# Kernel optimization log

Hardware: AMD Instinct MI355X
Metric: run time of the kernel (lower is better)

The kernel has to match this reference:

```python
import jax, jax.numpy as jnp
import numpy as np

D_INP=36; D_MODEL=144; NHEAD=4; NHID=128; NLAYERS=2
MAX_LEN=215; D_STATIC=9; D_PE=16; N_CLASSES=2; B=128
D_OB=D_MODEL//D_INP; GCH=MAX_LEN*D_OB; D_TR=D_MODEL+D_PE; D_FINAL=D_TR+D_INP
_EI=np.stack(np.nonzero(np.ones((D_INP,D_INP),dtype=np.int64)))  # torch.nonzero(ones).T -> all pairs
SRC_N=jnp.asarray(_EI[0]); TGT_N=jnp.asarray(_EI[1]); N_EDGE=_EI.shape[1]


def setup_inputs():
    ks=jax.random.split(jax.random.key(0),40)
    def w(i,shape,s=0.05): return jax.random.normal(ks[i],shape,jnp.float32)*s
    return {
      'src': jax.random.normal(ks[0],(MAX_LEN,B,2*D_INP),jnp.float32),
      'static': jax.random.normal(ks[1],(B,D_STATIC),jnp.float32),
      'times': jax.random.uniform(ks[2],(MAX_LEN,B),jnp.float32)*MAX_LEN,
      'lengths': jax.random.randint(ks[3],(B,),32,MAX_LEN+1),
      'R_u': w(4,(1,D_INP*D_OB)),
      'emb_w': w(5,(D_INP,D_STATIC)), 'emb_b': jnp.zeros(D_INP,jnp.float32),
      'Wv1': w(6,(GCH,GCH),1.0/np.sqrt(GCH)), 'bv1': jnp.zeros(GCH,jnp.float32),
      'Wv2': w(7,(GCH,GCH),1.0/np.sqrt(GCH)), 'bv2': jnp.zeros(GCH,jnp.float32),
      'in_proj_w': w(8,(NLAYERS,3*D_TR,D_TR)), 'in_proj_b': jnp.zeros((NLAYERS,3*D_TR),jnp.float32),
      'out_w': w(9,(NLAYERS,D_TR,D_TR)), 'out_b': jnp.zeros((NLAYERS,D_TR),jnp.float32),
      'lin1_w': w(10,(NLAYERS,NHID,D_TR)), 'lin1_b': jnp.zeros((NLAYERS,NHID),jnp.float32),
      'lin2_w': w(11,(NLAYERS,D_TR,NHID)), 'lin2_b': jnp.zeros((NLAYERS,D_TR),jnp.float32),
      'ln1_s': jnp.ones((NLAYERS,D_TR),jnp.float32), 'ln1_b': jnp.zeros((NLAYERS,D_TR),jnp.float32),
      'ln2_s': jnp.ones((NLAYERS,D_TR),jnp.float32), 'ln2_b': jnp.zeros((NLAYERS,D_TR),jnp.float32),
      'mlp1_w': w(12,(D_FINAL,D_FINAL)), 'mlp1_b': jnp.zeros(D_FINAL,jnp.float32),
      'mlp2_w': w(13,(N_CLASSES,D_FINAL)), 'mlp2_b': jnp.zeros(N_CLASSES,jnp.float32),
    }


def _seg_softmax(wgt, seg, n):
    m=jnp.full((n,),-jnp.inf,wgt.dtype).at[seg].max(wgt)
    e=jnp.exp(wgt-m[seg])
    s=jnp.zeros((n,),wgt.dtype).at[seg].add(e)
    return e/s[seg]


def _ln(x,s,b):
    mu=jnp.mean(x,-1,keepdims=True); v=jnp.var(x,-1,keepdims=True)
    return (x-mu)/jnp.sqrt(v+1e-5)*s+b


def _forward(src, static, times, R_u, emb_w, emb_b, Wv1, bv1, Wv2, bv2, in_proj_w, in_proj_b, out_w, out_b, lin1_w, lin1_b, lin2_w, lin2_b, ln1_s, ln1_b, ln2_s, ln2_b, mlp1_w, mlp1_b, mlp2_w, mlp2_b, lengths):
    T,Bb=src.shape[0],src.shape[1]
    obs=src[:,:,:D_INP]                                  # drop mask half
    h=jax.nn.relu(jnp.repeat(obs,D_OB,axis=-1)*R_u)      # h_u = relu(x_u*R_u), [T,B,144]
    ts=jnp.asarray(MAX_LEN**np.linspace(0,1,D_PE//2),jnp.float32)
    scaled=times[:,:,None]/ts
    pe=jnp.concatenate([jnp.sin(scaled),jnp.cos(scaled)],-1)  # [T,B,16]
    emb=static@emb_w.T+emb_b                             # [B,36]
    # --- Observation_progation x2 (use_beta=False): gather-softmax-scatter per sensor graph ---
    xb=h.transpose(1,0,2).reshape(Bb,T,D_INP,D_OB).transpose(0,2,1,3).reshape(Bb,D_INP,GCH)
    ew=jnp.ones((N_EDGE,),jnp.float32)                   # adj=ones -> edge_weights=1
    gamma=_seg_softmax(ew,TGT_N,D_INP)                   # softmax over edges per target node
    def prop(x_,Wv,bv):
        V=jax.nn.relu(x_@Wv.T+bv)                        # relu(lin_value(x_j))
        msgs=V[:,SRC_N,:]*gamma[None,:,None]             # gather source features per edge
        return jnp.zeros_like(x_).at[:,TGT_N,:].add(msgs)  # scatter-add to targets
    x1=prop(xb,Wv1,bv1)
    x2=prop(x1,Wv2,bv2)                                  # layer2 uses alpha1 = raw edge_weights
    alpha=jnp.broadcast_to(ew[None,:],(Bb,N_EDGE))       # alpha_all.T
    sq=jnp.sum(alpha*alpha,1)
    d2=jnp.maximum(sq[:,None]+sq[None,:]-2.0*(alpha@alpha.T),0.0)
    distance=jnp.mean(jnp.sqrt(d2))
    out=x2.reshape(Bb,D_INP,T,D_OB).transpose(2,0,1,3).reshape(T,Bb,D_INP*D_OB)
    x=jnp.concatenate([out,pe],-1)                       # [T,B,160]
    mask=jnp.arange(T)[None,:]>=lengths[:,None]          # [B,T] True = padded
    hd=D_TR//NHEAD
    for l in range(NLAYERS):                             # torch post-norm TransformerEncoderLayer
        qkv=x@in_proj_w[l].T+in_proj_b[l]
        q,k,v=jnp.split(qkv,3,-1)
        def heads(t): return t.reshape(T,Bb,NHEAD,hd).transpose(1,2,0,3)  # [B,H,T,hd]
        sc=jnp.einsum('bhqd,bhkd->bhqk',heads(q),heads(k))/np.sqrt(hd)
        sc=jnp.where(mask[:,None,None,:],jnp.float32(-1e30),sc)
        o=jnp.einsum('bhqk,bhkd->bhqd',jax.nn.softmax(sc,-1),heads(v))
        o=o.transpose(2,0,1,3).reshape(T,Bb,D_TR)@out_w[l].T+out_b[l]
        x=_ln(x+o,ln1_s[l],ln1_b[l])
        ff=jax.nn.relu(x@lin1_w[l].T+lin1_b[l])@lin2_w[l].T+lin2_b[l]
        x=_ln(x+ff,ln2_s[l],ln2_b[l])
    valid=1.0-mask.T[:,:,None].astype(x.dtype)           # [T,B,1]
    agg=jnp.sum(x*valid,0)/(lengths[:,None].astype(x.dtype)+1.0)
    feat=jnp.concatenate([agg,emb],1)                    # [B,196]
    logits=jax.nn.relu(feat@mlp1_w.T+mlp1_b)@mlp2_w.T+mlp2_b
    return logits,distance


def reference(src, static, times, lengths, R_u, emb_w, emb_b, Wv1, bv1, Wv2, bv2, in_proj_w, in_proj_b, out_w, out_b, lin1_w, lin1_b, lin2_w, lin2_b, ln1_s, ln1_b, ln2_s, ln2_b, mlp1_w, mlp1_b, mlp2_w, mlp2_b):
    return _forward(src, static, times, R_u, emb_w, emb_b, Wv1, bv1, Wv2, bv2, in_proj_w, in_proj_b, out_w, out_b, lin1_w, lin1_b, lin2_w, lin2_b, ln1_s, ln1_b, ln2_s, ln2_b, mlp1_w, mlp1_b, mlp2_w, mlp2_b, lengths)
```

## Files before the change

### kernel.cpp

```cpp
#include <hip/hip_runtime.h>
#include <math.h>

#define T_LEN 215
#define TP    224
#define B_N   128
#define DINP  36
#define D_TR  160
#define HD    40
#define D_FIN 196
#define KPG   864
#define MROW  28672

typedef __attribute__((ext_vector_type(8))) short short8v;
typedef __attribute__((ext_vector_type(4))) float f32x4;

__device__ __forceinline__ ushort f2bf(float x) {
  union { float f; unsigned u; } c; c.f = x;
  unsigned r = c.u + 0x7fffu + ((c.u >> 16) & 1u);
  return (ushort)(r >> 16);
}
__device__ __forceinline__ float bf2f(ushort h) {
  union { unsigned u; float f; } c; c.u = ((unsigned)h) << 16;
  return c.f;
}

__global__ __launch_bounds__(256) void k_prep(const float* __restrict__ Wv1,
    const float* __restrict__ Wv2, const float* __restrict__ ipw, const float* __restrict__ ow,
    const float* __restrict__ l1w, const float* __restrict__ l2w,
    ushort* __restrict__ wv1b, ushort* __restrict__ wv2b, ushort* __restrict__ ipwb,
    ushort* __restrict__ owb, ushort* __restrict__ l1wb, ushort* __restrict__ l2wb,
    float* __restrict__ v2acc, float* __restrict__ featacc, ushort* __restrict__ obuf16) {
  int i = blockIdx.x * 256 + threadIdx.x;
  if (i < 746496) { int n = i / KPG, k = i % KPG;
    wv1b[i] = (n < 860 && k < 860) ? f2bf(Wv1[n * 860 + k]) : (ushort)0; return; }
  i -= 746496;
  if (i < 746496) { int n = i / KPG, k = i % KPG;
    wv2b[i] = (n < 860 && k < 860) ? f2bf(Wv2[n * 860 + k]) : (ushort)0; return; }
  i -= 746496;
  if (i < 153600) { ipwb[i] = f2bf(ipw[i]); return; }
  i -= 153600;
  if (i < 51200)  { owb[i] = f2bf(ow[i]); return; }
  i -= 51200;
  if (i < 40960)  { l1wb[i] = f2bf(l1w[i]); return; }
  i -= 40960;
  if (i < 40960)  { l2wb[i] = f2bf(l2w[i]); return; }
  i -= 40960;
  if (i < 110592) { v2acc[i] = 0.f; return; }
  i -= 110592;
  if (i < 25088)  { featacc[i] = 0.f; return; }
  i -= 25088;
  if (i < 184320) {
    int b = i / 1440, rem = i % 1440;
    int t = 215 + rem / 160, cc = rem % 160;
    obuf16[((size_t)b * TP + t) * D_TR + cc] = 0; return;
  }
}

__global__ __launch_bounds__(256) void k_xb16(const float* __restrict__ src,
    const float* __restrict__ R_u, ushort* __restrict__ xb16) {
  __shared__ float Ss[T_LEN * DINP];
  const int b = blockIdx.x, tid = threadIdx.x;
  for (int i = tid; i < T_LEN * DINP; i += 256) {
    int t = i / DINP, j = i - t * DINP;
    Ss[i] = src[((size_t)t * B_N + b) * 72 + j];
  }
  __syncthreads();
  for (int i = tid; i < DINP * T_LEN; i += 256) {
    int ii = i / T_LEN, t = i - ii * T_LEN;
    float v = Ss[t * DINP + ii];
    float4 r = ((const float4*)R_u)[ii];
    ushort4 o;
    o.x = f2bf(fmaxf(v * r.x, 0.f)); o.y = f2bf(fmaxf(v * r.y, 0.f));
    o.z = f2bf(fmaxf(v * r.z, 0.f)); o.w = f2bf(fmaxf(v * r.w, 0.f));
    ushort* row = xb16 + (size_t)(b * DINP + ii) * KPG;
    *(ushort4*)(row + 4 * t) = o;
    if (t == 0) { ushort4 z = {0, 0, 0, 0}; *(ushort4*)(row + 860) = z; }
  }
}

__global__ __launch_bounds__(256) void k_red_s1(const ushort* __restrict__ V1b, ushort* __restrict__ s1) {
  int idx = blockIdx.x * 256 + threadIdx.x;
  if (idx >= B_N * KPG) return;
  int b = idx / KPG, n = idx % KPG;
  float s = 0.f;
  if (n < 860) {
    #pragma unroll 4
    for (int i = 0; i < DINP; i++) s += bf2f(V1b[((size_t)b * DINP + i) * 860 + n]);
    s *= (1.0f / 36.0f);
  }
  s1[idx] = (n < 860) ? f2bf(s) : (ushort)0;
}

__global__ __launch_bounds__(256) void k_buildx(const float* __restrict__ v2acc,
    const float* __restrict__ bv2, const float* __restrict__ times,
    float* __restrict__ x, ushort* __restrict__ x16) {
  int idx = blockIdx.x * 256 + threadIdx.x;
  if (idx >= B_N * TP * 40) return;
  int c = idx % 40;
  int r = idx / 40;
  int t = r % TP, b = r / TP;
  float4 f = {0.f, 0.f, 0.f, 0.f};
  if (t < T_LEN) {
    if (c < 36) {
      float4 a = *(const float4*)&v2acc[(size_t)b * KPG + 4 * t];
      float4 bb = *(const float4*)&bv2[4 * t];
      f.x = fmaxf(a.x + bb.x, 0.f); f.y = fmaxf(a.y + bb.y, 0.f);
      f.z = fmaxf(a.z + bb.z, 0.f); f.w = fmaxf(a.w + bb.w, 0.f);
    } else {
      float tm = times[t * B_N + b];
      int j0 = (c - 36) * 4;
      bool is_sin = j0 < 8;
      int kb = j0 & 7;
      float o[4];
      #pragma unroll
      for (int qq = 0; qq < 4; qq++) {
        float ts = expf((float)(kb + qq) * 0.76723400f);
        float sc = tm / ts;
        o[qq] = is_sin ? sinf(sc) : cosf(sc);
      }
      f.x = o[0]; f.y = o[1]; f.z = o[2]; f.w = o[3];
    }
  }
  ((float4*)(x + (size_t)r * D_TR))[c] = f;
  ushort4 h = {f2bf(f.x), f2bf(f.y), f2bf(f.z), f2bf(f.w)};
  *(ushort4*)(x16 + (size_t)r * D_TR + 4 * c) = h;
}

template <int RELU, int SPLIT, int WMODE, int BNT>
__global__ __launch_bounds__(256) void gemm_bf16(const ushort* __restrict__ A,
    const ushort* __restrict__ W, const float* __restrict__ bias, void* __restrict__ Cv,
    int KP, int ldc, int ncols, int kts) {
  __shared__ ushort As[128 * 32];
  __shared__ ushort Ws[BNT * 32];
  constexpr int NJ = BNT / 16;
  const int tid = threadIdx.x;
  const int wave = tid >> 6, lane = tid & 63;
  const int lr = lane & 15, hi = lane >> 4;
  const int m0 = blockIdx.y * 128, n0 = blockIdx.x * BNT;
  const int kt0 = blockIdx.z * kts;

  f32x4 acc[2][NJ];
  #pragma unroll
  for (int i = 0; i < 2; i++)
    #pragma unroll
    for (int j = 0; j < NJ; j++) acc[i][j] = (f32x4){0.f, 0.f, 0.f, 0.f};

  const int ar = tid >> 2, g = tid & 3;
  const size_t abase0 = (size_t)(m0 + ar) * KP;
  const size_t abase1 = (size_t)(m0 + ar + 64) * KP;
  const size_t bbase0 = (size_t)(n0 + ar) * KP;
  const size_t bbase1 = (size_t)(n0 + ar + 64) * KP;
  const int awb0 = ar * 64 + ((g * 16) ^ ((ar & 3) << 4));
  const int awb1 = awb0 + 64 * 64;

  const int arow0 = wave * 32 + lr;
  const int arb0 = arow0 * 64 + ((hi * 16) ^ ((arow0 & 3) << 4));
  const int arb1 = (arow0 + 16) * 64 + ((hi * 16) ^ (((arow0 + 16) & 3) << 4));
  int brb[NJ];
  #pragma unroll
  for (int j = 0; j < NJ; j++)
    brb[j] = (j * 16 + lr) * 64 + ((hi * 16) ^ ((lr & 3) << 4));

  for (int kt = 0; kt < kts; ++kt) {
    const int k0 = (kt0 + kt) * 32;
    uint4 va0 = *(const uint4*)(A + abase0 + k0 + g * 8);
    uint4 va1 = *(const uint4*)(A + abase1 + k0 + g * 8);
    uint4 vb0 = *(const uint4*)(W + bbase0 + k0 + g * 8);
    uint4 vb1;
    if constexpr (BNT == 128) vb1 = *(const uint4*)(W + bbase1 + k0 + g * 8);
    if (kt) __syncthreads();
    *(uint4*)((char*)As + awb0) = va0;
    *(uint4*)((char*)As + awb1) = va1;
    *(uint4*)((char*)Ws + awb0) = vb0;
    if constexpr (BNT == 128) *(uint4*)((char*)Ws + awb1) = vb1;
    __syncthreads();
    short8v a0 = *(const short8v*)((const char*)As + arb0);
    short8v a1 = *(const short8v*)((const char*)As + arb1);
    #pragma unroll
    for (int j = 0; j < NJ; j++) {
      short8v bf = *(const short8v*)((const char*)Ws + brb[j]);
      acc[0][j] = __builtin_amdgcn_mfma_f32_16x16x32_bf16(a0, bf, acc[0][j], 0, 0, 0);
      acc[1][j] = __builtin_amdgcn_mfma_f32_16x16x32_bf16(a1, bf, acc[1][j], 0, 0, 0);
    }
  }

  #pragma unroll
  for (int i = 0; i < 2; i++) {
    #pragma unroll
    for (int j = 0; j < NJ; j++) {
      int col = n0 + j * 16 + lr;
      int row = m0 + wave * 32 + i * 16 + hi * 4;
      if (col < ncols) {
        if (SPLIT) {
          #pragma unroll
          for (int r = 0; r < 4; r++)
            atomicAdd((float*)Cv + (size_t)(row + r) * ldc + col, acc[i][j][r]);
        } else {
          float bb = bias ? bias[col] : 0.f;
          #pragma unroll
          for (int r = 0; r < 4; r++) {
            float xv = acc[i][j][r] + bb;
            if (RELU) xv = fmaxf(xv, 0.f);
            if (WMODE == 0) ((float*)Cv)[(size_t)(row + r) * ldc + col] = xv;
            else            ((ushort*)Cv)[(size_t)(row + r) * ldc + col] = f2bf(xv);
          }
        }
      }
    }
  }
}

__global__ __launch_bounds__(256) void gemm_qkv(const ushort* __restrict__ A,
    const ushort* __restrict__ W, const float* __restrict__ bias,
    ushort* __restrict__ qkvB, ushort* __restrict__ Vt, int kts) {
  __shared__ ushort As[128 * 32];
  __shared__ ushort Ws[128 * 32];
  const int KP = 160;
  const int tid = threadIdx.x;
  const int wave = tid >> 6, lane = tid & 63;
  const int lr = lane & 15, hi = lane >> 4;
  const int m0 = blockIdx.y * 128, n0 = blockIdx.x * 128;

  f32x4 acc[2][8];
  #pragma unroll
  for (int i = 0; i < 2; i++)
    #pragma unroll
    for (int j = 0; j < 8; j++) acc[i][j] = (f32x4){0.f, 0.f, 0.f, 0.f};

  const int ar = tid >> 2, g = tid & 3;
  const size_t abase0 = (size_t)(m0 + ar) * KP;
  const size_t abase1 = (size_t)(m0 + ar + 64) * KP;
  const size_t bbase0 = (size_t)(n0 + ar) * KP;
  const size_t bbase1 = (size_t)(n0 + ar + 64) * KP;
  const int awb0 = ar * 64 + ((g * 16) ^ ((ar & 3) << 4));
  const int awb1 = awb0 + 64 * 64;

  const int arow0 = wave * 32 + lr;
  const int arb0 = arow0 * 64 + ((hi * 16) ^ ((arow0 & 3) << 4));
  const int arb1 = (arow0 + 16) * 64 + ((hi * 16) ^ (((arow0 + 16) & 3) << 4));
  int brb[8];
  #pragma unroll
  for (int j = 0; j < 8; j++)
    brb[j] = (j * 16 + lr) * 64 + ((hi * 16) ^ ((lr & 3) << 4));

  for (int kt = 0; kt < kts; ++kt) {
    const int k0 = kt * 32;
    uint4 va0 = *(const uint4*)(A + abase0 + k0 + g * 8);
    uint4 va1 = *(const uint4*)(A + abase1 + k0 + g * 8);
    uint4 vb0 = *(const uint4*)(W + bbase0 + k0 + g * 8);
    uint4 vb1 = *(const uint4*)(W + bbase1 + k0 + g * 8);
    if (kt) __syncthreads();
    *(uint4*)((char*)As + awb0) = va0;
    *(uint4*)((char*)As + awb1) = va1;
    *(uint4*)((char*)Ws + awb0) = vb0;
    *(uint4*)((char*)Ws + awb1) = vb1;
    __syncthreads();
    short8v a0 = *(const short8v*)((const char*)As + arb0);
    short8v a1 = *(const short8v*)((const char*)As + arb1);
    #pragma unroll
    for (int j = 0; j < 8; j++) {
      short8v bf = *(const short8v*)((const char*)Ws + brb[j]);
      acc[0][j] = __builtin_amdgcn_mfma_f32_16x16x32_bf16(a0, bf, acc[0][j], 0, 0, 0);
      acc[1][j] = __builtin_amdgcn_mfma_f32_16x16x32_bf16(a1, bf, acc[1][j], 0, 0, 0);
    }
  }

  #pragma unroll
  for (int i = 0; i < 2; i++) {
    const int row = m0 + wave * 32 + i * 16 + hi * 4;
    const int b = row / TP, t0 = row - b * TP;
    #pragma unroll
    for (int j = 0; j < 8; j++) {
      int col = n0 + j * 16 + lr;
      if (col < 320) {
        float bb = bias[col];
        #pragma unroll
        for (int r = 0; r < 4; r++)
          qkvB[(size_t)(row + r) * 480 + col] = f2bf(acc[i][j][r] + bb);
      } else if (col < 480) {
        float bb = bias[col];
        int dg = col - 320;
        int hh = dg / 40, dd = dg - hh * 40;
        ushort4 pv;
        pv.x = f2bf(acc[i][j][0] + bb); pv.y = f2bf(acc[i][j][1] + bb);
        pv.z = f2bf(acc[i][j][2] + bb); pv.w = f2bf(acc[i][j][3] + bb);
        *(ushort4*)(Vt + (((size_t)(b * 4 + hh) * 48 + dd) * TP + t0)) = pv;
      }
    }
  }
}

__global__ __launch_bounds__(256) void gemm_ln(const ushort* __restrict__ A,
    const ushort* __restrict__ W, const float* __restrict__ bias,
    const float* __restrict__ gam, const float* __restrict__ bet,
    float* __restrict__ x, ushort* __restrict__ x16, int KP, int kts) {
  __shared__ ushort As[64 * 32];
  __shared__ ushort Ws[160 * 32];
  const int tid = threadIdx.x;
  const int wave = tid >> 6, lane = tid & 63;
  const int lr = lane & 15, hi = lane >> 4;
  const int m0 = blockIdx.x * 64;

  f32x4 acc[10];
  #pragma unroll
  for (int j = 0; j < 10; j++) acc[j] = (f32x4){0.f, 0.f, 0.f, 0.f};

  const int ar = tid >> 2, g = tid & 3;
  const size_t abase = (size_t)(m0 + ar) * KP;
  const int awb = ar * 64 + ((g * 16) ^ ((ar & 3) << 4));
  const int wr0 = tid >> 2,         ws0 = tid & 3;
  const int wr1 = (tid + 256) >> 2, ws1 = (tid + 256) & 3;
  const int wr2 = (tid + 512) >> 2, ws2 = (tid + 512) & 3;
  const int wwb0 = wr0 * 64 + ((ws0 * 16) ^ ((wr0 & 3) << 4));
  const int wwb1 = wr1 * 64 + ((ws1 * 16) ^ ((wr1 & 3) << 4));
  const int wwb2 = wr2 * 64 + ((ws2 * 16) ^ ((wr2 & 3) << 4));

  const int arow = wave * 16 + lr;
  const int arb = arow * 64 + ((hi * 16) ^ ((arow & 3) << 4));
  int brb[10];
  #pragma unroll
  for (int j = 0; j < 10; j++)
    brb[j] = (j * 16 + lr) * 64 + ((hi * 16) ^ ((lr & 3) << 4));

  for (int kt = 0; kt < kts; ++kt) {
    const int k0 = kt * 32;
    uint4 va = *(const uint4*)(A + abase + k0 + g * 8);
    uint4 w0 = *(const uint4*)(W + (size_t)wr0 * KP + k0 + ws0 * 8);
    uint4 w1 = *(const uint4*)(W + (size_t)wr1 * KP + k0 + ws1 * 8);
    uint4 w2;
    if (tid < 128) w2 = *(const uint4*)(W + (size_t)wr2 * KP + k0 + ws2 * 8);
    if (kt) __syncthreads();
    *(uint4*)((char*)As + awb) = va;
    *(uint4*)((char*)Ws + wwb0) = w0;
    *(uint4*)((char*)Ws + wwb1) = w1;
    if (tid < 128) *(uint4*)((char*)Ws + wwb2) = w2;
    __syncthreads();
    short8v a0 = *(const short8v*)((const char*)As + arb);
    #pragma unroll
    for (int j = 0; j < 10; j++) {
      short8v bf = *(const short8v*)((const char*)Ws + brb[j]);
      acc[j] = __builtin_amdgcn_mfma_f32_16x16x32_bf16(a0, bf, acc[j], 0, 0, 0);
    }
  }

  const int rb = m0 + wave * 16 + hi * 4;
  float s[4] = {0.f, 0.f, 0.f, 0.f};
  #pragma unroll
  for (int j = 0; j < 10; j++) {
    const int col = j * 16 + lr;
    const float bb = bias[col];
    #pragma unroll
    for (int r = 0; r < 4; r++) {
      float v = acc[j][r] + bb + x[(size_t)(rb + r) * D_TR + col];
      acc[j][r] = v;
      s[r] += v;
    }
  }
  #pragma unroll
  for (int r = 0; r < 4; r++) {
    s[r] += __shfl_xor(s[r], 1, 64);
    s[r] += __shfl_xor(s[r], 2, 64);
    s[r] += __shfl_xor(s[r], 4, 64);
    s[r] += __shfl_xor(s[r], 8, 64);
  }
  float mu[4], q2[4] = {0.f, 0.f, 0.f, 0.f};
  #pragma unroll
  for (int r = 0; r < 4; r++) mu[r] = s[r] * (1.0f / 160.0f);
  #pragma unroll
  for (int j = 0; j < 10; j++)
    #pragma unroll
    for (int r = 0; r < 4; r++) {
      float d = acc[j][r] - mu[r];
      q2[r] += d * d;
    }
  #pragma unroll
  for (int r = 0; r < 4; r++) {
    q2[r] += __shfl_xor(q2[r], 1, 64);
    q2[r] += __shfl_xor(q2[r], 2, 64);
    q2[r] += __shfl_xor(q2[r], 4, 64);
    q2[r] += __shfl_xor(q2[r], 8, 64);
  }
  float rstd[4];
  #pragma unroll
  for (int r = 0; r < 4; r++) rstd[r] = rsqrtf(q2[r] * (1.0f / 160.0f) + 1e-5f);
  #pragma unroll
  for (int j = 0; j < 10; j++) {
    const int col = j * 16 + lr;
    const float gc = gam[col], bc = bet[col];
    #pragma unroll
    for (int r = 0; r < 4; r++) {
      float o = (acc[j][r] - mu[r]) * rstd[r] * gc + bc;
      x[(size_t)(rb + r) * D_TR + col] = o;
      x16[(size_t)(rb + r) * D_TR + col] = f2bf(o);
    }
  }
}

__global__ __launch_bounds__(64) void k_attn4(const ushort* __restrict__ qkvB,
    const ushort* __restrict__ Vt, const int* __restrict__ lengths,
    ushort* __restrict__ o16) {
  __shared__ ushort SP[16 * 232];
  const int bh = blockIdx.x;
  const int b = bh >> 2, h = bh & 3;
  int L = lengths[b]; if (L > T_LEN) L = T_LEN;
  const int q0 = blockIdx.y << 4;
  if (q0 >= L) return;
  const int lane = threadIdx.x;
  const int lr = lane & 15, hi = lane >> 4;
  const int nk16 = (L + 15) >> 4;
  const int nkt  = (L + 31) >> 5;
  const float SC = 0.15811388300841898f;

  const ushort* qrow = qkvB + ((size_t)b * TP + q0) * 480 + h * 40;
  uint4 qa0u = *(const uint4*)(qrow + lr * 480 + hi * 8);
  uint4 qa1u = {0, 0, 0, 0};
  if (hi == 0) qa1u = *(const uint4*)(qrow + lr * 480 + 32);
  short8v qa0 = *(short8v*)&qa0u;
  short8v qa1 = *(short8v*)&qa1u;

  f32x4 c[14];
  #pragma unroll
  for (int kt = 0; kt < 14; ++kt) {
    c[kt] = (f32x4){0.f, 0.f, 0.f, 0.f};
    if (kt < nk16) {
      const ushort* krow = qkvB + ((size_t)b * TP + kt * 16) * 480 + 160 + h * 40;
      uint4 kb0u = *(const uint4*)(krow + lr * 480 + hi * 8);
      uint4 kb1u = {0, 0, 0, 0};
      if (hi == 0) kb1u = *(const uint4*)(krow + lr * 480 + 32);
      c[kt] = __builtin_amdgcn_mfma_f32_16x16x32_bf16(qa0, *(short8v*)&kb0u, c[kt], 0, 0, 0);
      c[kt] = __builtin_amdgcn_mfma_f32_16x16x32_bf16(qa1, *(short8v*)&kb1u, c[kt], 0, 0, 0);
    }
  }

  float mx[4] = {-1e30f, -1e30f, -1e30f, -1e30f};
  #pragma unroll
  for (int kt = 0; kt < 14; ++kt) {
    if (kt < nk16) {
      bool valid = (kt * 16 + lr) < L;
      #pragma unroll
      for (int r = 0; r < 4; r++) {
        float v = valid ? c[kt][r] : -1e30f;
        mx[r] = fmaxf(mx[r], v);
      }
    }
  }
  #pragma unroll
  for (int r = 0; r < 4; r++) {
    mx[r] = fmaxf(mx[r], __shfl_xor(mx[r], 1, 64));
    mx[r] = fmaxf(mx[r], __shfl_xor(mx[r], 2, 64));
    mx[r] = fmaxf(mx[r], __shfl_xor(mx[r], 4, 64));
    mx[r] = fmaxf(mx[r], __shfl_xor(mx[r], 8, 64));
  }
  float sum[4] = {0.f, 0.f, 0.f, 0.f};
  #pragma unroll
  for (int kt = 0; kt < 14; ++kt) {
    if (kt < nk16) {
      bool valid = (kt * 16 + lr) < L;
      #pragma unroll
      for (int r = 0; r < 4; r++) {
        float p = valid ? __expf(SC * (c[kt][r] - mx[r])) : 0.f;
        sum[r] += p;
        c[kt][r] = p;
      }
    }
  }
  #pragma unroll
  for (int r = 0; r < 4; r++) {
    sum[r] += __shfl_xor(sum[r], 1, 64);
    sum[r] += __shfl_xor(sum[r], 2, 64);
    sum[r] += __shfl_xor(sum[r], 4, 64);
    sum[r] += __shfl_xor(sum[r], 8, 64);
  }

  const int nk16w = nkt * 2;
  #pragma unroll
  for (int kt = 0; kt < 14; ++kt) {
    if (kt < nk16w) {
      #pragma unroll
      for (int r = 0; r < 4; r++)
        SP[(hi * 4 + r) * 232 + kt * 16 + lr] = f2bf(c[kt][r]);
    }
  }
  __syncthreads();

  f32x4 o0 = {0.f, 0.f, 0.f, 0.f}, o1 = o0, o2 = o0;
  const ushort* vbase = Vt + (size_t)bh * 48 * TP;
  #pragma unroll
  for (int kt = 0; kt < 7; ++kt) {
    if (kt < nkt) {
      short8v pa = *(const short8v*)((const char*)SP + lr * 464 + kt * 64 + hi * 16);
      const ushort* vb = vbase + kt * 32 + hi * 8;
      short8v v0 = *(const short8v*)(vb + (size_t)lr * TP);
      short8v v1 = *(const short8v*)(vb + (size_t)(16 + lr) * TP);
      short8v v2 = *(const short8v*)(vb + (size_t)(32 + lr) * TP);
      o0 = __builtin_amdgcn_mfma_f32_16x16x32_bf16(pa, v0, o0, 0, 0, 0);
      o1 = __builtin_amdgcn_mfma_f32_16x16x32_bf16(pa, v1, o1, 0, 0, 0);
      o2 = __builtin_amdgcn_mfma_f32_16x16x32_bf16(pa, v2, o2, 0, 0, 0);
    }
  }

  #pragma unroll
  for (int r = 0; r < 4; r++) {
    int t = q0 + hi * 4 + r;
    if (t < T_LEN) {
      float inv = 1.0f / sum[r];
      ushort* op = o16 + ((size_t)b * TP + t) * D_TR + h * 40;
      op[lr]      = f2bf(o0[r] * inv);
      op[16 + lr] = f2bf(o1[r] * inv);
      if (lr < 8) op[32 + lr] = f2bf(o2[r] * inv);
    }
  }
}

__global__ __launch_bounds__(256) void k_agg(const float* __restrict__ x,
    const int* __restrict__ lengths, const float* __restrict__ stat,
    const float* __restrict__ emb_w, const float* __restrict__ emb_b,
    float* __restrict__ featacc) {
  const int cx = blockIdx.x, b = blockIdx.y;
  const int tid = threadIdx.x;
  int L = lengths[b]; if (L > T_LEN) L = T_LEN;
  const int c0 = cx * 27;
  if (tid < D_TR) {
    float s = 0.f;
    #pragma unroll
    for (int tl = 0; tl < 27; ++tl) {
      int t = c0 + tl;
      if (t < L) s += x[((size_t)b * TP + t) * D_TR + tid];
    }
    atomicAdd(&featacc[b * D_FIN + tid], s);
  } else if (cx == 0 && tid < D_FIN) {
    int i = tid - D_TR;
    float s = emb_b[i];
    #pragma unroll
    for (int k = 0; k < 9; k++) s = fmaf(stat[b * 9 + k], emb_w[i * 9 + k], s);
    featacc[b * D_FIN + tid] = s;
  }
}

__global__ __launch_bounds__(256) void k_mlp1(const float* __restrict__ featacc,
    const int* __restrict__ lengths, const float* __restrict__ m1w,
    const float* __restrict__ m1b, float* __restrict__ m1o) {
  const int b = blockIdx.y;
  const int wv = threadIdx.x >> 6, lane = threadIdx.x & 63;
  const int n = blockIdx.x * 4 + wv;
  int L = lengths[b]; if (L > T_LEN) L = T_LEN;
  const float inv = 1.0f / (float)(L + 1);
  const float* wr = m1w + (size_t)n * D_FIN;
  const float* fr = featacc + (size_t)b * D_FIN;
  float s = 0.f;
  for (int k = lane; k < D_FIN; k += 64) {
    float f = fr[k] * (k < D_TR ? inv : 1.f);
    s = fmaf(f, wr[k], s);
  }
  #pragma unroll
  for (int off = 32; off; off >>= 1) s += __shfl_xor(s, off, 64);
  if (lane == 0) m1o[(size_t)b * D_FIN + n] = fmaxf(s + m1b[n], 0.f);
}

__global__ __launch_bounds__(128) void k_logits(const float* __restrict__ m1o,
    const float* __restrict__ m2w, const float* __restrict__ m2b, float* __restrict__ out) {
  const int b = blockIdx.x;
  const int c = threadIdx.x >> 6, lane = threadIdx.x & 63;
  const float* mr = m1o + (size_t)b * D_FIN;
  const float* wr = m2w + c * D_FIN;
  float s = 0.f;
  for (int k = lane; k < D_FIN; k += 64) s = fmaf(mr[k], wr[k], s);
  #pragma unroll
  for (int off = 32; off; off >>= 1) s += __shfl_xor(s, off, 64);
  if (lane == 0) out[2 * b + c] = s + m2b[c];
  if (b == 0 && threadIdx.x == 127) out[256] = 0.f;
}

extern "C" void kernel_launch(void* const* d_in, const int* in_sizes, int n_in,
                              void* d_out, int out_size, void* d_ws, size_t ws_size,
                              hipStream_t stream) {
  const float* src   = (const float*)d_in[0];
  const float* stat  = (const float*)d_in[1];
  const float* times = (const float*)d_in[2];
  const int*   lens  = (const int*)d_in[3];
  const float* R_u   = (const float*)d_in[4];
  const float* emb_w = (const float*)d_in[5];
  const float* emb_b = (const float*)d_in[6];
  const float* Wv1   = (const float*)d_in[7];
  const float* bv1   = (const float*)d_in[8];
  const float* Wv2   = (const float*)d_in[9];
  const float* bv2   = (const float*)d_in[10];
  const float* ipw   = (const float*)d_in[11];
  const float* ipb   = (const float*)d_in[12];
  const float* ow    = (const float*)d_in[13];
  const float* ob    = (const float*)d_in[14];
  const float* l1w   = (const float*)d_in[15];
  const float* l1b   = (const float*)d_in[16];
  const float* l2w   = (const float*)d_in[17];
  const float* l2b   = (const float*)d_in[18];
  const float* ln1s  = (const float*)d_in[19];
  const float* ln1bb = (const float*)d_in[20];
  const float* ln2s  = (const float*)d_in[21];
  const float* ln2bb = (const float*)d_in[22];
  const float* m1w   = (const float*)d_in[23];
  const float* m1b   = (const float*)d_in[24];
  const float* m2w   = (const float*)d_in[25];
  const float* m2b   = (const float*)d_in[26];
  float* out = (float*)d_out;

  char* p = (char*)d_ws;
  float*  x      = (float*)p;   p += 18350080;
  ushort* x16    = (ushort*)p;  p += 9175040;
  float*  v2acc  = (float*)p;   p += 442368;
  ushort* s1b    = (ushort*)p;  p += 221184;
  ushort* obuf16 = (ushort*)p;  p += 9175040;
  ushort* wv1b   = (ushort*)p;  p += 1492992;
  ushort* wv2b   = (ushort*)p;  p += 1492992;
  ushort* ipwb   = (ushort*)p;  p += 307200;
  ushort* owb    = (ushort*)p;  p += 102400;
  ushort* l1wb   = (ushort*)p;  p += 81920;
  ushort* l2wb   = (ushort*)p;  p += 81920;
  float*  featacc= (float*)p;   p += 100352;
  float*  m1o    = (float*)p;   p += 100352;
  char*   R2     = p;
  ushort* xb16   = (ushort*)R2;
  ushort* V1b    = (ushort*)(R2 + 7962624);
  ushort* qkvB   = (ushort*)R2;
  ushort* ffb16  = (ushort*)R2;
  ushort* Vt     = (ushort*)(R2 + 27525120);

  k_prep<<<8202, 256, 0, stream>>>(Wv1, Wv2, ipw, ow, l1w, l2w,
                                   wv1b, wv2b, ipwb, owb, l1wb, l2wb, v2acc, featacc, obuf16);
  k_xb16<<<128, 256, 0, stream>>>(src, R_u, xb16);

  gemm_bf16<1, 0, 1, 128><<<dim3(7, 36, 1), 256, 0, stream>>>(
      xb16, wv1b, bv1, V1b, KPG, 860, 860, 27);
  k_red_s1<<<432, 256, 0, stream>>>(V1b, s1b);
  gemm_bf16<0, 1, 0, 64><<<dim3(14, 1, 9), 256, 0, stream>>>(
      s1b, wv2b, nullptr, v2acc, KPG, KPG, KPG, 3);
  k_buildx<<<4480, 256, 0, stream>>>(v2acc, bv2, times, x, x16);

  for (int l = 0; l < 2; l++) {
    gemm_qkv<<<dim3(4, 224, 1), 256, 0, stream>>>(
        x16, ipwb + (size_t)l * 76800, ipb + l * 480, qkvB, Vt, 5);
    k_attn4<<<dim3(512, 14), 64, 0, stream>>>(qkvB, Vt, lens, obuf16);
    gemm_ln<<<448, 256, 0, stream>>>(obuf16, owb + (size_t)l * 25600, ob + l * 160,
                                     ln1s + l * 160, ln1bb + l * 160, x, x16, 160, 5);
    gemm_bf16<1, 0, 1, 64><<<dim3(2, 224, 1), 256, 0, stream>>>(
        x16, l1wb + (size_t)l * 20480, l1b + l * 128, ffb16, 160, 128, 128, 5);
    gemm_ln<<<448, 256, 0, stream>>>(ffb16, l2wb + (size_t)l * 20480, l2b + l * 160,
                                     ln2s + l * 160, ln2bb + l * 160, x, x16, 128, 4);
  }

  k_agg<<<dim3(8, 128), 256, 0, stream>>>(x, lens, stat, emb_w, emb_b, featacc);
  k_mlp1<<<dim3(49, 128), 256, 0, stream>>>(featacc, lens, m1w, m1b, m1o);
  k_logits<<<128, 128, 0, stream>>>(m1o, m2w, m2b, out);
}
```

Before: 254.1 us.

## Drop fp32 residual stream, fuse aggregation into final LN, merge head kernels

The fp32 copy of the activation stream x is removed, so residuals are read back from the bf16 x16 buffer. This cuts memory traffic in gemm_ln and buildx, at the cost of accumulating residuals in bf16 precision. The masked time-sum aggregation is folded into the last gemm_ln epilogue through atomics, and the static embedding moves into the prep kernel. The xb16 kernel is merged into prep as extra blocks, and mlp1 plus logits become a single per-batch kernel, which removes several launches.

```diff
diff --git a/kernel.cpp b/kernel.cpp
--- a/kernel.cpp
+++ b/kernel.cpp
@@ -9,7 +9,6 @@
 #define HD    40
 #define D_FIN 196
 #define KPG   864
-#define MROW  28672
 
 typedef __attribute__((ext_vector_type(8))) short short8v;
 typedef __attribute__((ext_vector_type(4))) float f32x4;
@@ -27,9 +26,33 @@
 __global__ __launch_bounds__(256) void k_prep(const float* __restrict__ Wv1,
     const float* __restrict__ Wv2, const float* __restrict__ ipw, const float* __restrict__ ow,
     const float* __restrict__ l1w, const float* __restrict__ l2w,
+    const float* __restrict__ src, const float* __restrict__ R_u,
+    const float* __restrict__ stat, const float* __restrict__ emb_w, const float* __restrict__ emb_b,
     ushort* __restrict__ wv1b, ushort* __restrict__ wv2b, ushort* __restrict__ ipwb,
     ushort* __restrict__ owb, ushort* __restrict__ l1wb, ushort* __restrict__ l2wb,
-    float* __restrict__ v2acc, float* __restrict__ featacc, ushort* __restrict__ obuf16) {
+    float* __restrict__ v2acc, float* __restrict__ featacc, ushort* __restrict__ obuf16,
+    ushort* __restrict__ xb16) {
+  __shared__ float Ss[T_LEN * DINP];
+  if (blockIdx.x >= 8202) {
+    const int b = blockIdx.x - 8202, tid = threadIdx.x;
+    for (int i = tid; i < T_LEN * DINP; i += 256) {
+      int t = i / DINP, j = i - t * DINP;
+      Ss[i] = src[((size_t)t * B_N + b) * 72 + j];
+    }
+    __syncthreads();
+    for (int i = tid; i < DINP * T_LEN; i += 256) {
+      int ii = i / T_LEN, t = i - ii * T_LEN;
+      float v = Ss[t * DINP + ii];
+      float4 r = ((const float4*)R_u)[ii];
+      ushort4 o;
+      o.x = f2bf(fmaxf(v * r.x, 0.f)); o.y = f2bf(fmaxf(v * r.y, 0.f));
+      o.z = f2bf(fmaxf(v * r.z, 0.f)); o.w = f2bf(fmaxf(v * r.w, 0.f));
+      ushort* row = xb16 + (size_t)(b * DINP + ii) * KPG;
+      *(ushort4*)(row + 4 * t) = o;
+      if (t == 0) { ushort4 z = {0, 0, 0, 0}; *(ushort4*)(row + 860) = z; }
+    }
+    return;
+  }
   int i = blockIdx.x * 256 + threadIdx.x;
   if (i < 746496) { int n = i / KPG, k = i % KPG;
     wv1b[i] = (n < 860 && k < 860) ? f2bf(Wv1[n * 860 + k]) : (ushort)0; return; }
@@ -47,34 +70,19 @@
   i -= 40960;
   if (i < 110592) { v2acc[i] = 0.f; return; }
   i -= 110592;
-  if (i < 25088)  { featacc[i] = 0.f; return; }
-  i -= 25088;
+  if (i < 20480)  { int b = i / D_TR, d = i - b * D_TR;
+    featacc[b * D_FIN + d] = 0.f; return; }
+  i -= 20480;
+  if (i < 4608)   { int b = i / DINP, ii = i - b * DINP;
+    float s = emb_b[ii];
+    #pragma unroll
+    for (int k = 0; k < 9; k++) s = fmaf(stat[b * 9 + k], emb_w[ii * 9 + k], s);
+    featacc[b * D_FIN + D_TR + ii] = s; return; }
+  i -= 4608;
   if (i < 184320) {
     int b = i / 1440, rem = i % 1440;
     int t = 215 + rem / 160, cc = rem % 160;
     obuf16[((size_t)b * TP + t) * D_TR + cc] = 0; return;
-  }
-}
-
-__global__ __launch_bounds__(256) void k_xb16(const float* __restrict__ src,
-    const float* __restrict__ R_u, ushort* __restrict__ xb16) {
-  __shared__ float Ss[T_LEN * DINP];
-  const int b = blockIdx.x, tid = threadIdx.x;
-  for (int i = tid; i < T_LEN * DINP; i += 256) {
-    int t = i / DINP, j = i - t * DINP;
-    Ss[i] = src[((size_t)t * B_N + b) * 72 + j];
-  }
-  __syncthreads();
-  for (int i = tid; i < DINP * T_LEN; i += 256) {
-    int ii = i / T_LEN, t = i - ii * T_LEN;
-    float v = Ss[t * DINP + ii];
-    float4 r = ((const float4*)R_u)[ii];
-    ushort4 o;
-    o.x = f2bf(fmaxf(v * r.x, 0.f)); o.y = f2bf(fmaxf(v * r.y, 0.f));
-    o.z = f2bf(fmaxf(v * r.z, 0.f)); o.w = f2bf(fmaxf(v * r.w, 0.f));
-    ushort* row = xb16 + (size_t)(b * DINP + ii) * KPG;
-    *(ushort4*)(row + 4 * t) = o;
-    if (t == 0) { ushort4 z = {0, 0, 0, 0}; *(ushort4*)(row + 860) = z; }
   }
 }
 
@@ -93,7 +101,7 @@
 
 __global__ __launch_bounds__(256) void k_buildx(const float* __restrict__ v2acc,
     const float* __restrict__ bv2, const float* __restrict__ times,
-    float* __restrict__ x, ushort* __restrict__ x16) {
+    ushort* __restrict__ x16) {
   int idx = blockIdx.x * 256 + threadIdx.x;
   if (idx >= B_N * TP * 40) return;
   int c = idx % 40;
@@ -121,7 +129,6 @@
       f.x = o[0]; f.y = o[1]; f.z = o[2]; f.w = o[3];
     }
   }
-  ((float4*)(x + (size_t)r * D_TR))[c] = f;
   ushort4 h = {f2bf(f.x), f2bf(f.y), f2bf(f.z), f2bf(f.w)};
   *(ushort4*)(x16 + (size_t)r * D_TR + 4 * c) = h;
 }
@@ -293,7 +300,8 @@
 __global__ __launch_bounds__(256) void gemm_ln(const ushort* __restrict__ A,
     const ushort* __restrict__ W, const float* __restrict__ bias,
     const float* __restrict__ gam, const float* __restrict__ bet,
-    float* __restrict__ x, ushort* __restrict__ x16, int KP, int kts) {
+    ushort* __restrict__ x16, int KP, int kts,
+    const int* __restrict__ lengths, float* __restrict__ featacc) {
   __shared__ ushort As[64 * 32];
   __shared__ ushort Ws[160 * 32];
   const int tid = threadIdx.x;
@@ -351,7 +359,7 @@
     const float bb = bias[col];
     #pragma unroll
     for (int r = 0; r < 4; r++) {
-      float v = acc[j][r] + bb + x[(size_t)(rb + r) * D_TR + col];
+      float v = acc[j][r] + bb + bf2f(x16[(size_t)(rb + r) * D_TR + col]);
       acc[j][r] = v;
       s[r] += v;
     }
@@ -383,15 +391,32 @@
   float rstd[4];
   #pragma unroll
   for (int r = 0; r < 4; r++) rstd[r] = rsqrtf(q2[r] * (1.0f / 160.0f) + 1e-5f);
-  #pragma unroll
-  for (int j = 0; j < 10; j++) {
-    const int col = j * 16 + lr;
-    const float gc = gam[col], bc = bet[col];
-    #pragma unroll
-    for (int r = 0; r < 4; r++) {
-      float o = (acc[j][r] - mu[r]) * rstd[r] * gc + bc;
-      x[(size_t)(rb + r) * D_TR + col] = o;
-      x16[(size_t)(rb + r) * D_TR + col] = f2bf(o);
+
+  if (featacc == nullptr) {
+    #pragma unroll
+    for (int j = 0; j < 10; j++) {
+      const int col = j * 16 + lr;
+      const float gc = gam[col], bc = bet[col];
+      #pragma unroll
+      for (int r = 0; r < 4; r++) {
+        float o = (acc[j][r] - mu[r]) * rstd[r] * gc + bc;
+        x16[(size_t)(rb + r) * D_TR + col] = f2bf(o);
+      }
+    }
+  } else {
+    const int b = rb / TP, t0 = rb - b * TP;
+    int L = lengths[b]; if (L > T_LEN) L = T_LEN;
+    #pragma unroll
+    for (int j = 0; j < 10; j++) {
+      const int col = j * 16 + lr;
+      const float gc = gam[col], bc = bet[col];
+      float sacc = 0.f;
+      #pragma unroll
+      for (int r = 0; r < 4; r++) {
+        float o = (acc[j][r] - mu[r]) * rstd[r] * gc + bc;
+        if (t0 + r < L) sacc += o;
+      }
+      if (t0 < L) atomicAdd(&featacc[b * D_FIN + col], sacc);
     }
   }
 }
@@ -512,63 +537,43 @@
   }
 }
 
-__global__ __launch_bounds__(256) void k_agg(const float* __restrict__ x,
-    const int* __restrict__ lengths, const float* __restrict__ stat,
-    const float* __restrict__ emb_w, const float* __restrict__ emb_b,
-    float* __restrict__ featacc) {
-  const int cx = blockIdx.x, b = blockIdx.y;
-  const int tid = threadIdx.x;
-  int L = lengths[b]; if (L > T_LEN) L = T_LEN;
-  const int c0 = cx * 27;
-  if (tid < D_TR) {
-    float s = 0.f;
-    #pragma unroll
-    for (int tl = 0; tl < 27; ++tl) {
-      int t = c0 + tl;
-      if (t < L) s += x[((size_t)b * TP + t) * D_TR + tid];
-    }
-    atomicAdd(&featacc[b * D_FIN + tid], s);
-  } else if (cx == 0 && tid < D_FIN) {
-    int i = tid - D_TR;
-    float s = emb_b[i];
-    #pragma unroll
-    for (int k = 0; k < 9; k++) s = fmaf(stat[b * 9 + k], emb_w[i * 9 + k], s);
-    featacc[b * D_FIN + tid] = s;
-  }
-}
-
-__global__ __launch_bounds__(256) void k_mlp1(const float* __restrict__ featacc,
+__global__ __launch_bounds__(256) void k_head2(const float* __restrict__ featacc,
     const int* __restrict__ lengths, const float* __restrict__ m1w,
-    const float* __restrict__ m1b, float* __restrict__ m1o) {
-  const int b = blockIdx.y;
-  const int wv = threadIdx.x >> 6, lane = threadIdx.x & 63;
-  const int n = blockIdx.x * 4 + wv;
+    const float* __restrict__ m1b, const float* __restrict__ m2w,
+    const float* __restrict__ m2b, float* __restrict__ out) {
+  __shared__ float feat[196];
+  __shared__ float m1o_s[196];
+  __shared__ float r0[4], r1[4];
+  const int b = blockIdx.x, tid = threadIdx.x;
   int L = lengths[b]; if (L > T_LEN) L = T_LEN;
   const float inv = 1.0f / (float)(L + 1);
-  const float* wr = m1w + (size_t)n * D_FIN;
-  const float* fr = featacc + (size_t)b * D_FIN;
-  float s = 0.f;
-  for (int k = lane; k < D_FIN; k += 64) {
-    float f = fr[k] * (k < D_TR ? inv : 1.f);
-    s = fmaf(f, wr[k], s);
-  }
-  #pragma unroll
-  for (int off = 32; off; off >>= 1) s += __shfl_xor(s, off, 64);
-  if (lane == 0) m1o[(size_t)b * D_FIN + n] = fmaxf(s + m1b[n], 0.f);
-}
-
-__global__ __launch_bounds__(128) void k_logits(const float* __restrict__ m1o,
-    const float* __restrict__ m2w, const float* __restrict__ m2b, float* __restrict__ out) {
-  const int b = blockIdx.x;
-  const int c = threadIdx.x >> 6, lane = threadIdx.x & 63;
-  const float* mr = m1o + (size_t)b * D_FIN;
-  const float* wr = m2w + c * D_FIN;
-  float s = 0.f;
-  for (int k = lane; k < D_FIN; k += 64) s = fmaf(mr[k], wr[k], s);
-  #pragma unroll
-  for (int off = 32; off; off >>= 1) s += __shfl_xor(s, off, 64);
-  if (lane == 0) out[2 * b + c] = s + m2b[c];
-  if (b == 0 && threadIdx.x == 127) out[256] = 0.f;
+  if (tid < D_FIN)
+    feat[tid] = featacc[(size_t)b * D_FIN + tid] * (tid < D_TR ? inv : 1.f);
+  __syncthreads();
+  if (tid < D_FIN) {
+    float s = m1b[tid];
+    const float* wr = m1w + (size_t)tid * D_FIN;
+    #pragma unroll 4
+    for (int k = 0; k < D_FIN; k++) s = fmaf(feat[k], wr[k], s);
+    m1o_s[tid] = fmaxf(s, 0.f);
+  }
+  __syncthreads();
+  float p0 = 0.f, p1 = 0.f;
+  if (tid < D_FIN) {
+    p0 = m1o_s[tid] * m2w[tid];
+    p1 = m1o_s[tid] * m2w[D_FIN + tid];
+  }
+  #pragma unroll
+  for (int off = 32; off; off >>= 1) {
+    p0 += __shfl_xor(p0, off, 64);
+    p1 += __shfl_xor(p1, off, 64);
+  }
+  int w = tid >> 6;
+  if ((tid & 63) == 0) { r0[w] = p0; r1[w] = p1; }
+  __syncthreads();
+  if (tid == 0) out[2 * b]     = r0[0] + r0[1] + r0[2] + r0[3] + m2b[0];
+  if (tid == 1) out[2 * b + 1] = r1[0] + r1[1] + r1[2] + r1[3] + m2b[1];
+  if (b == 0 && tid == 2) out[256] = 0.f;
 }
 
 extern "C" void kernel_launch(void* const* d_in, const int* in_sizes, int n_in,
@@ -604,7 +609,6 @@
   float* out = (float*)d_out;
 
   char* p = (char*)d_ws;
-  float*  x      = (float*)p;   p += 18350080;
   ushort* x16    = (ushort*)p;  p += 9175040;
   float*  v2acc  = (float*)p;   p += 442368;
   ushort* s1b    = (ushort*)p;  p += 221184;
@@ -616,7 +620,6 @@
   ushort* l1wb   = (ushort*)p;  p += 81920;
   ushort* l2wb   = (ushort*)p;  p += 81920;
   float*  featacc= (float*)p;   p += 100352;
-  float*  m1o    = (float*)p;   p += 100352;
   char*   R2     = p;
   ushort* xb16   = (ushort*)R2;
   ushort* V1b    = (ushort*)(R2 + 7962624);
@@ -624,30 +627,31 @@
   ushort* ffb16  = (ushort*)R2;
   ushort* Vt     = (ushort*)(R2 + 27525120);
 
-  k_prep<<<8202, 256, 0, stream>>>(Wv1, Wv2, ipw, ow, l1w, l2w,
-                                   wv1b, wv2b, ipwb, owb, l1wb, l2wb, v2acc, featacc, obuf16);
-  k_xb16<<<128, 256, 0, stream>>>(src, R_u, xb16);
+  k_prep<<<8330, 256, 0, stream>>>(Wv1, Wv2, ipw, ow, l1w, l2w, src, R_u,
+                                   stat, emb_w, emb_b,
+                                   wv1b, wv2b, ipwb, owb, l1wb, l2wb,
+                                   v2acc, featacc, obuf16, xb16);
 
   gemm_bf16<1, 0, 1, 128><<<dim3(7, 36, 1), 256, 0, stream>>>(
       xb16, wv1b, bv1, V1b, KPG, 860, 860, 27);
   k_red_s1<<<432, 256, 0, stream>>>(V1b, s1b);
   gemm_bf16<0, 1, 0, 64><<<dim3(14, 1, 9), 256, 0, stream>>>(
       s1b, wv2b, nullptr, v2acc, KPG, KPG, KPG, 3);
-  k_buildx<<<4480, 256, 0, stream>>>(v2acc, bv2, times, x, x16);
+  k_buildx<<<4480, 256, 0, stream>>>(v2acc, bv2, times, x16);
 
   for (int l = 0; l < 2; l++) {
     gemm_qkv<<<dim3(4, 224, 1), 256, 0, stream>>>(
         x16, ipwb + (size_t)l * 76800, ipb + l * 480, qkvB, Vt, 5);
     k_attn4<<<dim3(512, 14), 64, 0, stream>>>(qkvB, Vt, lens, obuf16);
     gemm_ln<<<448, 256, 0, stream>>>(obuf16, owb + (size_t)l * 25600, ob + l * 160,
-                                     ln1s + l * 160, ln1bb + l * 160, x, x16, 160, 5);
+                                     ln1s + l * 160, ln1bb + l * 160, x16, 160, 5,
+                                     lens, nullptr);
     gemm_bf16<1, 0, 1, 64><<<dim3(2, 224, 1), 256, 0, stream>>>(
         x16, l1wb + (size_t)l * 20480, l1b + l * 128, ffb16, 160, 128, 128, 5);
     gemm_ln<<<448, 256, 0, stream>>>(ffb16, l2wb + (size_t)l * 20480, l2b + l * 160,
-                                     ln2s + l * 160, ln2bb + l * 160, x, x16, 128, 4);
-  }
-
-  k_agg<<<dim3(8, 128), 256, 0, stream>>>(x, lens, stat, emb_w, emb_b, featacc);
-  k_mlp1<<<dim3(49, 128), 256, 0, stream>>>(featacc, lens, m1w, m1b, m1o);
-  k_logits<<<128, 128, 0, stream>>>(m1o, m2w, m2b, out);
-}
+                                     ln2s + l * 160, ln2bb + l * 160, x16, 128, 4,
+                                     lens, (l == 1) ? featacc : nullptr);
+  }
+
+  k_head2<<<128, 256, 0, stream>>>(featacc, lens, m1w, m1b, m2w, m2b, out);
+}
```

Result: faster. 248.1 us (-2.3%).
